# Kernel optimization log

Hardware: AMD Instinct MI355X
Metric: run time of the kernel (lower is better)

The kernel has to match this reference:

```python
import jax, jax.numpy as jnp
import numpy as np

DIMS = 1024
VOCAB = 32000
BATCH = 128
SEQ = 512


def setup_inputs() -> dict:
    key = jax.random.key(0)
    ks = jax.random.split(key, 10)
    s = 1.0 / np.sqrt(DIMS)
    inp = {
        'features': jax.random.randint(ks[0], (BATCH, SEQ), 0, VOCAB, dtype=jnp.int32),
        'embeddings': jax.random.normal(ks[1], (VOCAB, DIMS), dtype=jnp.float32) * s,
        'Wf': jax.random.normal(ks[2], (DIMS, DIMS), dtype=jnp.float32) * s,
        'Uf': jax.random.normal(ks[3], (DIMS, DIMS), dtype=jnp.float32) * s,
        'bf': jnp.zeros((1, DIMS), dtype=jnp.float32),
        'Wi': jax.random.normal(ks[4], (DIMS, DIMS), dtype=jnp.float32) * s,
        'Ui': jax.random.normal(ks[5], (DIMS, DIMS), dtype=jnp.float32) * s,
        'bi': jnp.zeros((1, DIMS), dtype=jnp.float32),
        'Wo': jax.random.normal(ks[6], (DIMS, DIMS), dtype=jnp.float32) * s,
        'Uo': jax.random.normal(ks[7], (DIMS, DIMS), dtype=jnp.float32) * s,
        'bo': jnp.zeros((1, DIMS), dtype=jnp.float32),
        'Wc': jax.random.normal(ks[8], (DIMS, DIMS), dtype=jnp.float32) * s,
        'Uc': jax.random.normal(ks[9], (DIMS, DIMS), dtype=jnp.float32) * s,
        'bc': jnp.zeros((1, DIMS), dtype=jnp.float32),
    }
    return inp


def reference(features, embeddings, Wf, Uf, bf, Wi, Ui, bi, Wo, Uo, bo, Wc, Uc, bc):
    # Embedding lookup for all timesteps: (B, T, D) -> (T, B, D) for scan
    x = embeddings[features]  # (B, T, D)
    x = jnp.transpose(x, (1, 0, 2))  # (T, B, D)
    B = features.shape[0]
    h0 = jnp.zeros((B, DIMS), dtype=embeddings.dtype)
    c0 = jnp.zeros((B, DIMS), dtype=embeddings.dtype)

    def step(carry, xt):
        h, c = carry
        ft = jax.nn.sigmoid(xt @ Wf + h @ Uf + bf)
        ot = jax.nn.sigmoid(xt @ Wo + h @ Uo + bo)
        it = jax.nn.sigmoid(xt @ Wi + h @ Ui + bi)
        ct = jnp.tanh(xt @ Wc + h @ Uc + bc)
        c = ft * c + it * ct
        h = ot * jnp.tanh(c)
        return (h, c), None

    (h, c), _ = jax.lax.scan(step, (h0, c0), x)
    return jnp.concatenate([h, c], axis=1)  # (B, 2*D)
```

## Files before the change

kernel.cpp:

```cpp
#include <hip/hip_runtime.h>
#include <hip/hip_bf16.h>

#define DIMS 1024
#define SEQ 512
#define BATCH 128
#define VOCAB 32000
#define GRID 256

typedef __attribute__((ext_vector_type(8))) short short8;
typedef __attribute__((ext_vector_type(4))) float f32x4;

__device__ __forceinline__ ushort f2bf(float x) {
    union { float f; unsigned u; } v; v.f = x;
    unsigned u = v.u;
    return (ushort)((u + 0x7FFFu + ((u >> 16) & 1u)) >> 16);
}

__global__ void conv_emb_kernel(const float* __restrict__ in, ushort* __restrict__ out, int n) {
    int idx = blockIdx.x * blockDim.x + threadIdx.x;
    int stride = gridDim.x * blockDim.x;
    for (int i = idx * 4; i < n; i += stride * 4) {
        float4 v = *(const float4*)(in + i);
        ushort4 o;
        o.x = f2bf(v.x); o.y = f2bf(v.y); o.z = f2bf(v.z); o.w = f2bf(v.w);
        *(ushort4*)(out + i) = o;
    }
}

__launch_bounds__(512, 2)
__global__ void lstm_kernel(const int* __restrict__ feats,
                            const ushort* __restrict__ emb,
                            const float* __restrict__ Wf, const float* __restrict__ Uf, const float* __restrict__ bfp,
                            const float* __restrict__ Wi, const float* __restrict__ Ui, const float* __restrict__ bip,
                            const float* __restrict__ Wo, const float* __restrict__ Uo, const float* __restrict__ bop,
                            const float* __restrict__ Wc, const float* __restrict__ Uc, const float* __restrict__ bcp,
                            ushort* __restrict__ hbuf, float* __restrict__ out, int* __restrict__ flags) {
    __shared__ ushort Bl[32 * 2048];
    __shared__ float pre0[64 * 36];
    __shared__ float pre1[64 * 36];

    const int tid = threadIdx.x;
    const int bid = blockIdx.x;
    const int rg = bid >> 7;
    const int cb = bid & 127;

    for (int idx = tid; idx < 32 * 2048; idx += 512) {
        int cl = idx & 31;
        int k  = idx >> 5;
        int g  = cl >> 3, dd0 = cl & 7;
        int dw = cb * 8 + dd0;
        const float* Wg = (g == 0) ? Wf : (g == 1) ? Wi : (g == 2) ? Wo : Wc;
        const float* Ug = (g == 0) ? Uf : (g == 1) ? Ui : (g == 2) ? Uo : Uc;
        float v = (k < 1024) ? Wg[k * 1024 + dw] : Ug[(k - 1024) * 1024 + dw];
        int boff = ((cl << 12) | (k << 1)) ^ ((cl & 7) << 4);
        *(ushort*)((char*)Bl + boff) = f2bf(v);
    }

    const int lane = tid & 63;
    const int w  = tid >> 6;
    const int wr = w & 3;
    const int kh = w >> 2;
    const int lx = lane & 15;
    const int qq = lane >> 4;
    const int kg = qq * 8;
    const int lr = wr * 16 + lx;
    const int brow = rg * 64 + lr;

    const int bofs0 = (lx << 12) ^ ((lx & 7) << 4);
    const int bofs1 = ((16 + lx) << 12) ^ ((lx & 7) << 4);

    const int kb    = kh * 512;
    const int fbase = kh * 64;
    float* myPre = kh ? pre1 : pre0;
    const int r0 = wr * 16 + qq * 4;

    const int grow_ = tid >> 3;
    const int gdd   = tid & 7;
    const int gd    = cb * 8 + gdd;
    const float bF = bfp[gd], bI = bip[gd], bO = bop[gd], bC = bcp[gd];

    float cst = 0.f;
    int* myflags = flags + rg * 128;
    int fidx = feats[brow * SEQ];

    __syncthreads();

    for (int t = 0; t < SEQ; t++) {
        f32x4 a00 = {0,0,0,0}, a01 = {0,0,0,0};
        f32x4 a10 = {0,0,0,0}, a11 = {0,0,0,0};

        {
            const ushort* xrow = emb + (size_t)fidx * DIMS;
            fidx = (t + 1 < SEQ) ? feats[brow * SEQ + t + 1] : 0;
            #pragma unroll 4
            for (int ks = 0; ks < 16; ks += 2) {
                {
                    int k = kb + ks * 32 + kg;
                    short8 a  = *(const short8*)(xrow + k);
                    short8 b0 = *(const short8*)((const char*)Bl + (bofs0 ^ (k << 1)));
                    short8 b1 = *(const short8*)((const char*)Bl + (bofs1 ^ (k << 1)));
                    a00 = __builtin_amdgcn_mfma_f32_16x16x32_bf16(a, b0, a00, 0, 0, 0);
                    a10 = __builtin_amdgcn_mfma_f32_16x16x32_bf16(a, b1, a10, 0, 0, 0);
                }
                {
                    int k = kb + (ks + 1) * 32 + kg;
                    short8 a  = *(const short8*)(xrow + k);
                    short8 b0 = *(const short8*)((const char*)Bl + (bofs0 ^ (k << 1)));
                    short8 b1 = *(const short8*)((const char*)Bl + (bofs1 ^ (k << 1)));
                    a01 = __builtin_amdgcn_mfma_f32_16x16x32_bf16(a, b0, a01, 0, 0, 0);
                    a11 = __builtin_amdgcn_mfma_f32_16x16x32_bf16(a, b1, a11, 0, 0, 0);
                }
            }
        }

        if (t > 0) {
            long guard = 0;
            for (;;) {
                int f0 = __hip_atomic_load(myflags + fbase + lane, __ATOMIC_RELAXED, __HIP_MEMORY_SCOPE_AGENT);
                if (__all(f0 >= t)) break;
                __builtin_amdgcn_s_sleep(1);
                if (++guard > 100000000L) break;
            }
            const ushort* hbase = hbuf + (size_t)((t & 1) * 2 + rg) * (128 * 512);
            #pragma unroll 4
            for (int ks = 0; ks < 16; ks += 2) {
                {
                    int chunk = fbase + ks * 4 + qq;
                    const unsigned long long* hp =
                        (const unsigned long long*)(hbase + (chunk << 9) + lr * 8);
                    union { unsigned long long u[2]; short8 v; } av;
                    av.u[0] = __hip_atomic_load(hp,     __ATOMIC_RELAXED, __HIP_MEMORY_SCOPE_AGENT);
                    av.u[1] = __hip_atomic_load(hp + 1, __ATOMIC_RELAXED, __HIP_MEMORY_SCOPE_AGENT);
                    int k = 1024 + kb + ks * 32 + kg;
                    short8 b0 = *(const short8*)((const char*)Bl + (bofs0 ^ (k << 1)));
                    short8 b1 = *(const short8*)((const char*)Bl + (bofs1 ^ (k << 1)));
                    a00 = __builtin_amdgcn_mfma_f32_16x16x32_bf16(av.v, b0, a00, 0, 0, 0);
                    a10 = __builtin_amdgcn_mfma_f32_16x16x32_bf16(av.v, b1, a10, 0, 0, 0);
                }
                {
                    int chunk = fbase + (ks + 1) * 4 + qq;
                    const unsigned long long* hp =
                        (const unsigned long long*)(hbase + (chunk << 9) + lr * 8);
                    union { unsigned long long u[2]; short8 v; } av;
                    av.u[0] = __hip_atomic_load(hp,     __ATOMIC_RELAXED, __HIP_MEMORY_SCOPE_AGENT);
                    av.u[1] = __hip_atomic_load(hp + 1, __ATOMIC_RELAXED, __HIP_MEMORY_SCOPE_AGENT);
                    int k = 1024 + kb + (ks + 1) * 32 + kg;
                    short8 b0 = *(const short8*)((const char*)Bl + (bofs0 ^ (k << 1)));
                    short8 b1 = *(const short8*)((const char*)Bl + (bofs1 ^ (k << 1)));
                    a01 = __builtin_amdgcn_mfma_f32_16x16x32_bf16(av.v, b0, a01, 0, 0, 0);
                    a11 = __builtin_amdgcn_mfma_f32_16x16x32_bf16(av.v, b1, a11, 0, 0, 0);
                }
            }
        }

        #pragma unroll
        for (int j = 0; j < 4; j++) {
            myPre[(r0 + j) * 36 + lx]      = a00[j] + a01[j];
            myPre[(r0 + j) * 36 + 16 + lx] = a10[j] + a11[j];
        }
        __syncthreads();

        {
            int base = grow_ * 36;
            float pf = pre0[base + gdd]      + pre1[base + gdd]      + bF;
            float pi = pre0[base + 8 + gdd]  + pre1[base + 8 + gdd]  + bI;
            float po = pre0[base + 16 + gdd] + pre1[base + 16 + gdd] + bO;
            float pc = pre0[base + 24 + gdd] + pre1[base + 24 + gdd] + bC;
            float f  = 1.f / (1.f + __expf(-pf));
            float ig = 1.f / (1.f + __expf(-pi));
            float o  = 1.f / (1.f + __expf(-po));
            float e2 = __expf(2.f * pc);
            float cc = (e2 - 1.f) / (e2 + 1.f);
            float cn = f * cst + ig * cc;
            cst = cn;
            float e2c = __expf(2.f * cn);
            float th  = (e2c - 1.f) / (e2c + 1.f);
            float h   = o * th;
            if (t < SEQ - 1) {
                ushort* hw = hbuf + (size_t)(((t + 1) & 1) * 2 + rg) * (128 * 512) + cb * 512 + tid;
                __hip_atomic_store(hw, f2bf(h), __ATOMIC_RELAXED, __HIP_MEMORY_SCOPE_AGENT);
            } else {
                int gr = rg * 64 + grow_;
                out[gr * 2048 + gd] = h;
                out[gr * 2048 + 1024 + gd] = cn;
            }
        }

        if (t < SEQ - 1) {
            asm volatile("s_waitcnt vmcnt(0)" ::: "memory");
            __syncthreads();
            if (tid == 0) {
                __hip_atomic_store(myflags + cb, t + 1, __ATOMIC_RELAXED, __HIP_MEMORY_SCOPE_AGENT);
            }
        }
    }
}

extern "C" void kernel_launch(void* const* d_in, const int* in_sizes, int n_in,
                              void* d_out, int out_size, void* d_ws, size_t ws_size,
                              hipStream_t stream) {
    const int*   feats = (const int*)d_in[0];
    const float* emb_f = (const float*)d_in[1];
    const float* Wf = (const float*)d_in[2];
    const float* Uf = (const float*)d_in[3];
    const float* bf_ = (const float*)d_in[4];
    const float* Wi = (const float*)d_in[5];
    const float* Ui = (const float*)d_in[6];
    const float* bi_ = (const float*)d_in[7];
    const float* Wo = (const float*)d_in[8];
    const float* Uo = (const float*)d_in[9];
    const float* bo_ = (const float*)d_in[10];
    const float* Wc = (const float*)d_in[11];
    const float* Uc = (const float*)d_in[12];
    const float* bc_ = (const float*)d_in[13];

    char* ws = (char*)d_ws;
    ushort* emb_bf = (ushort*)ws;
    ushort* hbuf   = (ushort*)(ws + 65536000);
    int*    flags  = (int*)(ws + 65536000 + 524288);

    hipMemsetAsync(flags, 0, 1024, stream);
    conv_emb_kernel<<<1024, 256, 0, stream>>>(emb_f, emb_bf, VOCAB * DIMS);
    lstm_kernel<<<GRID, 512, 0, stream>>>(feats, emb_bf,
                                          Wf, Uf, bf_, Wi, Ui, bi_,
                                          Wo, Uo, bo_, Wc, Uc, bc_,
                                          hbuf, (float*)d_out, flags);
}
```

Measured before the change: 4.032 ms.

## Split K four ways per wave with two row tiles and LDS atomic reduction

Warps are reorganised so each wave covers two 16-row tiles and a quarter of the K range, reusing each B fragment read from shared memory across two row tiles. This halves the LDS B-fragment reads per MFMA. Partial sums are reduced with shared-memory atomicAdd into a double-buffered pre-activation array that is zeroed for the next step. The cost is four-way atomic contention in LDS and an extra zeroing pass each timestep.

Result: slower. 9.074 ms (+125.1%).

```diff
diff --git a/kernel.cpp b/kernel.cpp
--- a/kernel.cpp
+++ b/kernel.cpp
@@ -36,8 +36,7 @@
                             const float* __restrict__ Wc, const float* __restrict__ Uc, const float* __restrict__ bcp,
                             ushort* __restrict__ hbuf, float* __restrict__ out, int* __restrict__ flags) {
     __shared__ ushort Bl[32 * 2048];
-    __shared__ float pre0[64 * 36];
-    __shared__ float pre1[64 * 36];
+    __shared__ float pre[2][64 * 36];
 
     const int tid = threadIdx.x;
     const int bid = blockIdx.x;
@@ -55,24 +54,23 @@
         int boff = ((cl << 12) | (k << 1)) ^ ((cl & 7) << 4);
         *(ushort*)((char*)Bl + boff) = f2bf(v);
     }
+    for (int i = tid; i < 64 * 36; i += 512) { pre[0][i] = 0.f; pre[1][i] = 0.f; }
 
     const int lane = tid & 63;
     const int w  = tid >> 6;
-    const int wr = w & 3;
-    const int kh = w >> 2;
+    const int rh = w & 1;
+    const int kq = w >> 1;
     const int lx = lane & 15;
     const int qq = lane >> 4;
     const int kg = qq * 8;
-    const int lr = wr * 16 + lx;
-    const int brow = rg * 64 + lr;
+    const int kqb = kq * 256;
+    const int rowA = rh * 32 + lx;
+    const int rowB = rowA + 16;
+    const int browA = rg * 64 + rowA;
+    const int browB = rg * 64 + rowB;
 
     const int bofs0 = (lx << 12) ^ ((lx & 7) << 4);
     const int bofs1 = ((16 + lx) << 12) ^ ((lx & 7) << 4);
-
-    const int kb    = kh * 512;
-    const int fbase = kh * 64;
-    float* myPre = kh ? pre1 : pre0;
-    const int r0 = wr * 16 + qq * 4;
 
     const int grow_ = tid >> 3;
     const int gdd   = tid & 7;
@@ -81,91 +79,91 @@
 
     float cst = 0.f;
     int* myflags = flags + rg * 128;
-    int fidx = feats[brow * SEQ];
+    const int fpoll = kq * 32 + (lane & 31);
+    int fidxA = feats[browA * SEQ];
+    int fidxB = feats[browB * SEQ];
 
     __syncthreads();
 
     for (int t = 0; t < SEQ; t++) {
-        f32x4 a00 = {0,0,0,0}, a01 = {0,0,0,0};
-        f32x4 a10 = {0,0,0,0}, a11 = {0,0,0,0};
+        f32x4 a00 = {0,0,0,0};
+        f32x4 a01 = {0,0,0,0};
+        f32x4 a10 = {0,0,0,0};
+        f32x4 a11 = {0,0,0,0};
 
         {
-            const ushort* xrow = emb + (size_t)fidx * DIMS;
-            fidx = (t + 1 < SEQ) ? feats[brow * SEQ + t + 1] : 0;
-            #pragma unroll 4
-            for (int ks = 0; ks < 16; ks += 2) {
-                {
-                    int k = kb + ks * 32 + kg;
-                    short8 a  = *(const short8*)(xrow + k);
-                    short8 b0 = *(const short8*)((const char*)Bl + (bofs0 ^ (k << 1)));
-                    short8 b1 = *(const short8*)((const char*)Bl + (bofs1 ^ (k << 1)));
-                    a00 = __builtin_amdgcn_mfma_f32_16x16x32_bf16(a, b0, a00, 0, 0, 0);
-                    a10 = __builtin_amdgcn_mfma_f32_16x16x32_bf16(a, b1, a10, 0, 0, 0);
-                }
-                {
-                    int k = kb + (ks + 1) * 32 + kg;
-                    short8 a  = *(const short8*)(xrow + k);
-                    short8 b0 = *(const short8*)((const char*)Bl + (bofs0 ^ (k << 1)));
-                    short8 b1 = *(const short8*)((const char*)Bl + (bofs1 ^ (k << 1)));
-                    a01 = __builtin_amdgcn_mfma_f32_16x16x32_bf16(a, b0, a01, 0, 0, 0);
-                    a11 = __builtin_amdgcn_mfma_f32_16x16x32_bf16(a, b1, a11, 0, 0, 0);
-                }
+            const ushort* xrowA = emb + (size_t)fidxA * DIMS;
+            const ushort* xrowB = emb + (size_t)fidxB * DIMS;
+            if (t + 1 < SEQ) {
+                fidxA = feats[browA * SEQ + t + 1];
+                fidxB = feats[browB * SEQ + t + 1];
+            }
+            #pragma unroll
+            for (int ks = 0; ks < 8; ks++) {
+                int k = kqb + ks * 32 + kg;
+                short8 aA = *(const short8*)(xrowA + k);
+                short8 aB = *(const short8*)(xrowB + k);
+                short8 b0 = *(const short8*)((const char*)Bl + (bofs0 ^ (k << 1)));
+                short8 b1 = *(const short8*)((const char*)Bl + (bofs1 ^ (k << 1)));
+                a00 = __builtin_amdgcn_mfma_f32_16x16x32_bf16(aA, b0, a00, 0, 0, 0);
+                a01 = __builtin_amdgcn_mfma_f32_16x16x32_bf16(aB, b0, a01, 0, 0, 0);
+                a10 = __builtin_amdgcn_mfma_f32_16x16x32_bf16(aA, b1, a10, 0, 0, 0);
+                a11 = __builtin_amdgcn_mfma_f32_16x16x32_bf16(aB, b1, a11, 0, 0, 0);
             }
         }
 
         if (t > 0) {
             long guard = 0;
             for (;;) {
-                int f0 = __hip_atomic_load(myflags + fbase + lane, __ATOMIC_RELAXED, __HIP_MEMORY_SCOPE_AGENT);
+                int f0 = __hip_atomic_load(myflags + fpoll, __ATOMIC_RELAXED, __HIP_MEMORY_SCOPE_AGENT);
                 if (__all(f0 >= t)) break;
                 __builtin_amdgcn_s_sleep(1);
                 if (++guard > 100000000L) break;
             }
             const ushort* hbase = hbuf + (size_t)((t & 1) * 2 + rg) * (128 * 512);
-            #pragma unroll 4
-            for (int ks = 0; ks < 16; ks += 2) {
-                {
-                    int chunk = fbase + ks * 4 + qq;
-                    const unsigned long long* hp =
-                        (const unsigned long long*)(hbase + (chunk << 9) + lr * 8);
-                    union { unsigned long long u[2]; short8 v; } av;
-                    av.u[0] = __hip_atomic_load(hp,     __ATOMIC_RELAXED, __HIP_MEMORY_SCOPE_AGENT);
-                    av.u[1] = __hip_atomic_load(hp + 1, __ATOMIC_RELAXED, __HIP_MEMORY_SCOPE_AGENT);
-                    int k = 1024 + kb + ks * 32 + kg;
-                    short8 b0 = *(const short8*)((const char*)Bl + (bofs0 ^ (k << 1)));
-                    short8 b1 = *(const short8*)((const char*)Bl + (bofs1 ^ (k << 1)));
-                    a00 = __builtin_amdgcn_mfma_f32_16x16x32_bf16(av.v, b0, a00, 0, 0, 0);
-                    a10 = __builtin_amdgcn_mfma_f32_16x16x32_bf16(av.v, b1, a10, 0, 0, 0);
-                }
-                {
-                    int chunk = fbase + (ks + 1) * 4 + qq;
-                    const unsigned long long* hp =
-                        (const unsigned long long*)(hbase + (chunk << 9) + lr * 8);
-                    union { unsigned long long u[2]; short8 v; } av;
-                    av.u[0] = __hip_atomic_load(hp,     __ATOMIC_RELAXED, __HIP_MEMORY_SCOPE_AGENT);
-                    av.u[1] = __hip_atomic_load(hp + 1, __ATOMIC_RELAXED, __HIP_MEMORY_SCOPE_AGENT);
-                    int k = 1024 + kb + (ks + 1) * 32 + kg;
-                    short8 b0 = *(const short8*)((const char*)Bl + (bofs0 ^ (k << 1)));
-                    short8 b1 = *(const short8*)((const char*)Bl + (bofs1 ^ (k << 1)));
-                    a01 = __builtin_amdgcn_mfma_f32_16x16x32_bf16(av.v, b0, a01, 0, 0, 0);
-                    a11 = __builtin_amdgcn_mfma_f32_16x16x32_bf16(av.v, b1, a11, 0, 0, 0);
-                }
-            }
-        }
-
-        #pragma unroll
-        for (int j = 0; j < 4; j++) {
-            myPre[(r0 + j) * 36 + lx]      = a00[j] + a01[j];
-            myPre[(r0 + j) * 36 + 16 + lx] = a10[j] + a11[j];
+            #pragma unroll
+            for (int ks = 0; ks < 8; ks++) {
+                int chunk = kq * 32 + ks * 4 + qq;
+                const unsigned long long* hpA =
+                    (const unsigned long long*)(hbase + (chunk << 9) + rowA * 8);
+                const unsigned long long* hpB =
+                    (const unsigned long long*)(hbase + (chunk << 9) + rowB * 8);
+                union { unsigned long long u[2]; short8 v; } avA, avB;
+                avA.u[0] = __hip_atomic_load(hpA,     __ATOMIC_RELAXED, __HIP_MEMORY_SCOPE_AGENT);
+                avA.u[1] = __hip_atomic_load(hpA + 1, __ATOMIC_RELAXED, __HIP_MEMORY_SCOPE_AGENT);
+                avB.u[0] = __hip_atomic_load(hpB,     __ATOMIC_RELAXED, __HIP_MEMORY_SCOPE_AGENT);
+                avB.u[1] = __hip_atomic_load(hpB + 1, __ATOMIC_RELAXED, __HIP_MEMORY_SCOPE_AGENT);
+                int k = 1024 + kqb + ks * 32 + kg;
+                short8 b0 = *(const short8*)((const char*)Bl + (bofs0 ^ (k << 1)));
+                short8 b1 = *(const short8*)((const char*)Bl + (bofs1 ^ (k << 1)));
+                a00 = __builtin_amdgcn_mfma_f32_16x16x32_bf16(avA.v, b0, a00, 0, 0, 0);
+                a01 = __builtin_amdgcn_mfma_f32_16x16x32_bf16(avB.v, b0, a01, 0, 0, 0);
+                a10 = __builtin_amdgcn_mfma_f32_16x16x32_bf16(avA.v, b1, a10, 0, 0, 0);
+                a11 = __builtin_amdgcn_mfma_f32_16x16x32_bf16(avB.v, b1, a11, 0, 0, 0);
+            }
+        }
+
+        {
+            float* P = pre[t & 1];
+            #pragma unroll
+            for (int j = 0; j < 4; j++) {
+                int rA = rh * 32 + qq * 4 + j;
+                int rB = rA + 16;
+                atomicAdd(&P[rA * 36 + lx],      a00[j]);
+                atomicAdd(&P[rB * 36 + lx],      a01[j]);
+                atomicAdd(&P[rA * 36 + 16 + lx], a10[j]);
+                atomicAdd(&P[rB * 36 + 16 + lx], a11[j]);
+            }
         }
         __syncthreads();
 
         {
+            const float* P = pre[t & 1];
             int base = grow_ * 36;
-            float pf = pre0[base + gdd]      + pre1[base + gdd]      + bF;
-            float pi = pre0[base + 8 + gdd]  + pre1[base + 8 + gdd]  + bI;
-            float po = pre0[base + 16 + gdd] + pre1[base + 16 + gdd] + bO;
-            float pc = pre0[base + 24 + gdd] + pre1[base + 24 + gdd] + bC;
+            float pf = P[base + gdd]      + bF;
+            float pi = P[base + 8 + gdd]  + bI;
+            float po = P[base + 16 + gdd] + bO;
+            float pc = P[base + 24 + gdd] + bC;
             float f  = 1.f / (1.f + __expf(-pf));
             float ig = 1.f / (1.f + __expf(-pi));
             float o  = 1.f / (1.f + __expf(-po));
@@ -176,6 +174,11 @@
             float e2c = __expf(2.f * cn);
             float th  = (e2c - 1.f) / (e2c + 1.f);
             float h   = o * th;
+
+            float* Pz = pre[(t + 1) & 1];
+            #pragma unroll
+            for (int i = tid; i < 64 * 36; i += 512) Pz[i] = 0.f;
+
             if (t < SEQ - 1) {
                 ushort* hw = hbuf + (size_t)(((t + 1) & 1) * 2 + rg) * (128 * 512) + cb * 512 + tid;
                 __hip_atomic_store(hw, f2bf(h), __ATOMIC_RELAXED, __HIP_MEMORY_SCOPE_AGENT);
```

## Fuse embedding bf16 conversion into LSTM and use deep rotating h buffer

Applied to the files above, without the earlier changes.

Removes the separate pass that converted the whole embedding table to bf16, converting each gathered fp32 row in registers with packed cvt instructions instead. The h exchange buffer becomes a 32-deep ring, and h is read with plain vector loads rather than pairs of relaxed atomic loads. This avoids a full-table conversion pass and cheapens the per-step h fetch. In exchange it doubles x-load bytes per step and relies on ring depth to avoid reading stale cached h values.

Result: slower. 6.394 ms (+58.6%).

```diff
diff --git a/kernel.cpp b/kernel.cpp
--- a/kernel.cpp
+++ b/kernel.cpp
@@ -6,6 +6,7 @@
 #define BATCH 128
 #define VOCAB 32000
 #define GRID 256
+#define HDEPTH 32
 
 typedef __attribute__((ext_vector_type(8))) short short8;
 typedef __attribute__((ext_vector_type(4))) float f32x4;
@@ -16,25 +17,27 @@
     return (ushort)((u + 0x7FFFu + ((u >> 16) & 1u)) >> 16);
 }
 
-__global__ void conv_emb_kernel(const float* __restrict__ in, ushort* __restrict__ out, int n) {
-    int idx = blockIdx.x * blockDim.x + threadIdx.x;
-    int stride = gridDim.x * blockDim.x;
-    for (int i = idx * 4; i < n; i += stride * 4) {
-        float4 v = *(const float4*)(in + i);
-        ushort4 o;
-        o.x = f2bf(v.x); o.y = f2bf(v.y); o.z = f2bf(v.z); o.w = f2bf(v.w);
-        *(ushort4*)(out + i) = o;
-    }
+__device__ __forceinline__ short8 pack8cvt(const float* p) {
+    float4 f0 = *(const float4*)p;
+    float4 f1 = *(const float4*)(p + 4);
+    int r0, r1, r2, r3;
+    asm("v_cvt_pk_bf16_f32 %0, %1, %2" : "=v"(r0) : "v"(f0.x), "v"(f0.y));
+    asm("v_cvt_pk_bf16_f32 %0, %1, %2" : "=v"(r1) : "v"(f0.z), "v"(f0.w));
+    asm("v_cvt_pk_bf16_f32 %0, %1, %2" : "=v"(r2) : "v"(f1.x), "v"(f1.y));
+    asm("v_cvt_pk_bf16_f32 %0, %1, %2" : "=v"(r3) : "v"(f1.z), "v"(f1.w));
+    union { int i[4]; short8 v; } u;
+    u.i[0] = r0; u.i[1] = r1; u.i[2] = r2; u.i[3] = r3;
+    return u.v;
 }
 
 __launch_bounds__(512, 2)
 __global__ void lstm_kernel(const int* __restrict__ feats,
-                            const ushort* __restrict__ emb,
+                            const float* __restrict__ emb,
                             const float* __restrict__ Wf, const float* __restrict__ Uf, const float* __restrict__ bfp,
                             const float* __restrict__ Wi, const float* __restrict__ Ui, const float* __restrict__ bip,
                             const float* __restrict__ Wo, const float* __restrict__ Uo, const float* __restrict__ bop,
                             const float* __restrict__ Wc, const float* __restrict__ Uc, const float* __restrict__ bcp,
-                            ushort* __restrict__ hbuf, float* __restrict__ out, int* __restrict__ flags) {
+                            ushort* __restrict__ hrot, float* __restrict__ out, int* __restrict__ flags) {
     __shared__ ushort Bl[32 * 2048];
     __shared__ float pre0[64 * 36];
     __shared__ float pre1[64 * 36];
@@ -90,13 +93,13 @@
         f32x4 a10 = {0,0,0,0}, a11 = {0,0,0,0};
 
         {
-            const ushort* xrow = emb + (size_t)fidx * DIMS;
+            const float* xrow = emb + (size_t)fidx * DIMS;
             fidx = (t + 1 < SEQ) ? feats[brow * SEQ + t + 1] : 0;
             #pragma unroll 4
             for (int ks = 0; ks < 16; ks += 2) {
                 {
                     int k = kb + ks * 32 + kg;
-                    short8 a  = *(const short8*)(xrow + k);
+                    short8 a  = pack8cvt(xrow + k);
                     short8 b0 = *(const short8*)((const char*)Bl + (bofs0 ^ (k << 1)));
                     short8 b1 = *(const short8*)((const char*)Bl + (bofs1 ^ (k << 1)));
                     a00 = __builtin_amdgcn_mfma_f32_16x16x32_bf16(a, b0, a00, 0, 0, 0);
@@ -104,7 +107,7 @@
                 }
                 {
                     int k = kb + (ks + 1) * 32 + kg;
-                    short8 a  = *(const short8*)(xrow + k);
+                    short8 a  = pack8cvt(xrow + k);
                     short8 b0 = *(const short8*)((const char*)Bl + (bofs0 ^ (k << 1)));
                     short8 b1 = *(const short8*)((const char*)Bl + (bofs1 ^ (k << 1)));
                     a01 = __builtin_amdgcn_mfma_f32_16x16x32_bf16(a, b0, a01, 0, 0, 0);
@@ -121,34 +124,26 @@
                 __builtin_amdgcn_s_sleep(1);
                 if (++guard > 100000000L) break;
             }
-            const ushort* hbase = hbuf + (size_t)((t & 1) * 2 + rg) * (128 * 512);
+            const ushort* hbase = hrot + (size_t)(t % HDEPTH) * (256 * 512) + (size_t)rg * (128 * 512);
             #pragma unroll 4
             for (int ks = 0; ks < 16; ks += 2) {
                 {
                     int chunk = fbase + ks * 4 + qq;
-                    const unsigned long long* hp =
-                        (const unsigned long long*)(hbase + (chunk << 9) + lr * 8);
-                    union { unsigned long long u[2]; short8 v; } av;
-                    av.u[0] = __hip_atomic_load(hp,     __ATOMIC_RELAXED, __HIP_MEMORY_SCOPE_AGENT);
-                    av.u[1] = __hip_atomic_load(hp + 1, __ATOMIC_RELAXED, __HIP_MEMORY_SCOPE_AGENT);
+                    short8 hv = *(const short8*)(hbase + (chunk << 9) + lr * 8);
                     int k = 1024 + kb + ks * 32 + kg;
                     short8 b0 = *(const short8*)((const char*)Bl + (bofs0 ^ (k << 1)));
                     short8 b1 = *(const short8*)((const char*)Bl + (bofs1 ^ (k << 1)));
-                    a00 = __builtin_amdgcn_mfma_f32_16x16x32_bf16(av.v, b0, a00, 0, 0, 0);
-                    a10 = __builtin_amdgcn_mfma_f32_16x16x32_bf16(av.v, b1, a10, 0, 0, 0);
+                    a00 = __builtin_amdgcn_mfma_f32_16x16x32_bf16(hv, b0, a00, 0, 0, 0);
+                    a10 = __builtin_amdgcn_mfma_f32_16x16x32_bf16(hv, b1, a10, 0, 0, 0);
                 }
                 {
                     int chunk = fbase + (ks + 1) * 4 + qq;
-                    const unsigned long long* hp =
-                        (const unsigned long long*)(hbase + (chunk << 9) + lr * 8);
-                    union { unsigned long long u[2]; short8 v; } av;
-                    av.u[0] = __hip_atomic_load(hp,     __ATOMIC_RELAXED, __HIP_MEMORY_SCOPE_AGENT);
-                    av.u[1] = __hip_atomic_load(hp + 1, __ATOMIC_RELAXED, __HIP_MEMORY_SCOPE_AGENT);
+                    short8 hv = *(const short8*)(hbase + (chunk << 9) + lr * 8);
                     int k = 1024 + kb + (ks + 1) * 32 + kg;
                     short8 b0 = *(const short8*)((const char*)Bl + (bofs0 ^ (k << 1)));
                     short8 b1 = *(const short8*)((const char*)Bl + (bofs1 ^ (k << 1)));
-                    a01 = __builtin_amdgcn_mfma_f32_16x16x32_bf16(av.v, b0, a01, 0, 0, 0);
-                    a11 = __builtin_amdgcn_mfma_f32_16x16x32_bf16(av.v, b1, a11, 0, 0, 0);
+                    a01 = __builtin_amdgcn_mfma_f32_16x16x32_bf16(hv, b0, a01, 0, 0, 0);
+                    a11 = __builtin_amdgcn_mfma_f32_16x16x32_bf16(hv, b1, a11, 0, 0, 0);
                 }
             }
         }
@@ -177,7 +172,7 @@
             float th  = (e2c - 1.f) / (e2c + 1.f);
             float h   = o * th;
             if (t < SEQ - 1) {
-                ushort* hw = hbuf + (size_t)(((t + 1) & 1) * 2 + rg) * (128 * 512) + cb * 512 + tid;
+                ushort* hw = hrot + (size_t)((t + 1) % HDEPTH) * (256 * 512) + (size_t)bid * 512 + tid;
                 __hip_atomic_store(hw, f2bf(h), __ATOMIC_RELAXED, __HIP_MEMORY_SCOPE_AGENT);
             } else {
                 int gr = rg * 64 + grow_;
@@ -215,14 +210,12 @@
     const float* bc_ = (const float*)d_in[13];
 
     char* ws = (char*)d_ws;
-    ushort* emb_bf = (ushort*)ws;
-    ushort* hbuf   = (ushort*)(ws + 65536000);
-    int*    flags  = (int*)(ws + 65536000 + 524288);
+    ushort* hrot  = (ushort*)ws;
+    int*    flags = (int*)(ws + 8388608);
 
     hipMemsetAsync(flags, 0, 1024, stream);
-    conv_emb_kernel<<<1024, 256, 0, stream>>>(emb_f, emb_bf, VOCAB * DIMS);
-    lstm_kernel<<<GRID, 512, 0, stream>>>(feats, emb_bf,
+    lstm_kernel<<<GRID, 512, 0, stream>>>(feats, emb_f,
                                           Wf, Uf, bf_, Wi, Ui, bi_,
                                           Wo, Uo, bo_, Wc, Uc, bc_,
-                                          hbuf, (float*)d_out, flags);
-}
+                                          hrot, (float*)d_out, flags);
+}
```
